# Kernel optimization log

Hardware: AMD Instinct MI355X
Metric: run time of the kernel (lower is better)

The kernel has to match this reference:

```python
import jax, jax.numpy as jnp
import numpy as np

N_NODES = 100000
N_EDGES = 3200000
D_FEAT = 128
N_LAYERS = 2

def setup_inputs() -> dict:
    key = jax.random.key(0)
    k1, k2, k3, k4 = jax.random.split(key, 4)
    x = jax.random.normal(k1, (N_NODES, D_FEAT), dtype=jnp.float32)
    edge_row = jax.random.randint(k2, (N_EDGES,), 0, N_NODES)  # destination (spmm output row)
    edge_col = jax.random.randint(k3, (N_EDGES,), 0, N_NODES)  # source node
    edge_vals = jax.random.uniform(k4, (N_EDGES,), dtype=jnp.float32)
    scalars = jnp.ones((N_LAYERS,), dtype=jnp.float32)  # per-layer learned scalar (init ones)
    return {"x": x, "edge_row": edge_row, "edge_col": edge_col,
            "edge_vals": edge_vals, "scalars": scalars}

def reference(x, edge_row, edge_col, edge_vals, scalars):
    # ScalarSGC forward with dropout p=0 (identity). Same adjacency each layer.
    for l in range(N_LAYERS):
        h = scalars[l] * x                      # scalar * x
        msg = edge_vals[:, None] * h[edge_col]  # [E, D] gather + scale
        agg = jax.ops.segment_sum(msg, edge_row, num_segments=N_NODES)  # spmm
        x = jax.nn.elu(agg)
    return x
```

## Files before the change

### kernel.cpp

```cpp
#include <hip/hip_runtime.h>
#include <math.h>
#include <stdint.h>


#define D_FEAT 128
#define D2     64
#define SCAN_TILE 1024

#define PB 256
#define PT 1024
#define RB_BITS 9
#define ROWS_PER_BUCKET 512
#define COL_BITS 17
#define CACHE_CAP 17152

__device__ __forceinline__ uint32_t f2bf(float f) {
    uint32_t u = __float_as_uint(f);
    return (u + 0x7FFFu + ((u >> 16) & 1u)) >> 16;
}
__device__ __forceinline__ float bf_lo(uint32_t w) { return __uint_as_float(w << 16); }
__device__ __forceinline__ float bf_hi(uint32_t w) { return __uint_as_float(w & 0xFFFF0000u); }

__global__ void convert_kernel(const float2* __restrict__ xin, uint32_t* __restrict__ xbf, int n2) {
    int i = blockIdx.x * blockDim.x + threadIdx.x;
    if (i < n2) {
        float2 f = xin[i];
        xbf[i] = f2bf(f.x) | (f2bf(f.y) << 16);
    }
}

__global__ __launch_bounds__(PT) void coarse_count_kernel(const int* __restrict__ row,
                                                          int* __restrict__ cnt,
                                                          int E, int nbuck) {
    __shared__ int hist[256];
    const int t = threadIdx.x;
    if (t < 256) hist[t] = 0;
    __syncthreads();
    const int stride = PB * PT;
    for (int i = blockIdx.x * PT + t; i < E; i += stride)
        atomicAdd(&hist[row[i] >> RB_BITS], 1);
    __syncthreads();
    if (t < nbuck) cnt[t * PB + blockIdx.x] = hist[t];
}

__global__ __launch_bounds__(SCAN_TILE) void scan1_kernel(const int* __restrict__ counts,
                                                          int* __restrict__ excl,
                                                          int* __restrict__ tileSums, int n) {
    __shared__ int wsum[16];
    const int tid  = threadIdx.x;
    const int lane = tid & 63;
    const int wave = tid >> 6;
    const int i    = blockIdx.x * SCAN_TILE + tid;

    int v = (i < n) ? counts[i] : 0;
    int incl = v;
    #pragma unroll
    for (int off = 1; off < 64; off <<= 1) {
        int t = __shfl_up(incl, off, 64);
        if (lane >= off) incl += t;
    }
    if (lane == 63) wsum[wave] = incl;
    __syncthreads();
    if (wave == 0) {
        int s = (lane < 16) ? wsum[lane] : 0;
        #pragma unroll
        for (int off = 1; off < 16; off <<= 1) {
            int t = __shfl_up(s, off, 64);
            if (lane >= off) s += t;
        }
        if (lane < 16) wsum[lane] = s;
    }
    __syncthreads();
    int wbase = (wave == 0) ? 0 : wsum[wave - 1];
    if (i < n) excl[i] = wbase + (incl - v);
    if (tid == 0) tileSums[blockIdx.x] = wsum[15];
}

__global__ __launch_bounds__(1024) void scan2_kernel(const int* __restrict__ tileSums,
                                                     int* __restrict__ tileBase,
                                                     int* __restrict__ total_out, int nb) {
    __shared__ int buf[1024];
    const int tid = threadIdx.x;
    int v = (tid < nb) ? tileSums[tid] : 0;
    buf[tid] = v;
    __syncthreads();
    #pragma unroll
    for (int off = 1; off < 1024; off <<= 1) {
        int t = (tid >= off) ? buf[tid - off] : 0;
        __syncthreads();
        buf[tid] += t;
        __syncthreads();
    }
    if (tid < nb) tileBase[tid] = buf[tid] - v;
    if (tid == nb - 1) *total_out = buf[tid];
}

__global__ __launch_bounds__(PT) void partition_kernel(const int* __restrict__ row,
                                                       const int* __restrict__ col,
                                                       const float* __restrict__ val,
                                                       const int* __restrict__ cnt,
                                                       const int* __restrict__ tileBase,
                                                       int2* __restrict__ pack2,
                                                       int E, int nbuck) {
    __shared__ int cur[256];
    const int t = threadIdx.x;
    if (t < nbuck) {
        int idx = t * PB + blockIdx.x;
        cur[t] = cnt[idx] + tileBase[idx >> 10];
    }
    __syncthreads();
    const int stride = PB * PT;
    for (int i = blockIdx.x * PT + t; i < E; i += stride) {
        int r = row[i];
        int pos = atomicAdd(&cur[r >> RB_BITS], 1);
        pack2[pos] = make_int2(col[i] | ((r & (ROWS_PER_BUCKET - 1)) << COL_BITS),
                               __float_as_int(val[i]));
    }
}

__global__ __launch_bounds__(1024) void fine_sort_kernel(const int* __restrict__ cnt,
                                                         const int* __restrict__ tileBase,
                                                         const int2* __restrict__ pack2,
                                                         int2* __restrict__ pack,
                                                         int* __restrict__ offsets,
                                                         int E, int N, int nbuck) {
    extern __shared__ int2 ecache[];
    __shared__ int buf[1024];
    __shared__ int cur[ROWS_PER_BUCKET];
    const int b = blockIdx.x;
    const int t = threadIdx.x;
    const int start = cnt[b << 8] + tileBase[b >> 2];
    const int end   = (b == nbuck - 1) ? E : (cnt[(b + 1) << 8] + tileBase[(b + 1) >> 2]);
    const int n  = end - start;
    const int nc = (n < CACHE_CAP) ? n : CACHE_CAP;

    for (int i = t; i < nc; i += 1024) ecache[i] = pack2[start + i];
    buf[t] = 0;
    __syncthreads();

    for (int i = t; i < n; i += 1024) {
        int key = (i < nc) ? ecache[i].x : pack2[start + i].x;
        atomicAdd(&buf[((unsigned)key) >> COL_BITS], 1);
    }
    __syncthreads();

    int v = buf[t];
    for (int off = 1; off < 1024; off <<= 1) {
        int tv = (t >= off) ? buf[t - off] : 0;
        __syncthreads();
        buf[t] += tv;
        __syncthreads();
    }
    int excl = buf[t] - v;
    if (t < ROWS_PER_BUCKET) {
        int r = (b << RB_BITS) + t;
        if (r < N) offsets[r] = start + excl;
        cur[t] = excl;
    }
    if (b == 0 && t == 0) offsets[N] = E;
    __syncthreads();

    for (int i = t; i < n; i += 1024) {
        int2 w = (i < nc) ? ecache[i] : pack2[start + i];
        int lr = ((unsigned)w.x) >> COL_BITS;
        int p = atomicAdd(&cur[lr], 1);
        pack[start + p] = make_int2(w.x & ((1 << COL_BITS) - 1), w.y);
    }
}

template <int OUT_BF16>
__global__ __launch_bounds__(256) void spmm_elu_kernel(
    const int* __restrict__ offsets, const int2* __restrict__ pack,
    const uint32_t* __restrict__ xin, void* __restrict__ xout,
    const float* __restrict__ scalars, int layer, int N) {
    const int tid = threadIdx.x;
    const int grp = tid >> 4;
    const int sub = tid & 15;
    const int r   = blockIdx.x * 16 + grp;

    int e = 0, end = 0;
    if (r < N) { e = offsets[r]; end = offsets[r + 1]; }

    const uint4* __restrict__ xin4 = (const uint4*)xin;

    float a[8];
    #pragma unroll
    for (int k = 0; k < 8; ++k) a[k] = 0.f;

    #define FMA8(W, V)                                                     \
        a[0] += (V) * bf_lo((W).x); a[1] += (V) * bf_hi((W).x);            \
        a[2] += (V) * bf_lo((W).y); a[3] += (V) * bf_hi((W).y);            \
        a[4] += (V) * bf_lo((W).z); a[5] += (V) * bf_hi((W).z);            \
        a[6] += (V) * bf_lo((W).w); a[7] += (V) * bf_hi((W).w);

    for (; e + 4 <= end; e += 4) {
        int2 p0 = pack[e], p1 = pack[e + 1], p2 = pack[e + 2], p3 = pack[e + 3];
        uint4 w0 = xin4[(((uint32_t)p0.x) << 4) + sub];
        uint4 w1 = xin4[(((uint32_t)p1.x) << 4) + sub];
        uint4 w2 = xin4[(((uint32_t)p2.x) << 4) + sub];
        uint4 w3 = xin4[(((uint32_t)p3.x) << 4) + sub];
        FMA8(w0, __int_as_float(p0.y));
        FMA8(w1, __int_as_float(p1.y));
        FMA8(w2, __int_as_float(p2.y));
        FMA8(w3, __int_as_float(p3.y));
    }
    for (; e < end; ++e) {
        int2 p = pack[e];
        uint4 w = xin4[(((uint32_t)p.x) << 4) + sub];
        FMA8(w, __int_as_float(p.y));
    }
    #undef FMA8

    const float s = scalars[layer];
    #pragma unroll
    for (int k = 0; k < 8; ++k) {
        float x = a[k] * s;
        a[k] = (x > 0.f) ? x : (expf(x) - 1.f);
    }

    if (r < N) {
        if (OUT_BF16) {
            uint4 o;
            o.x = f2bf(a[0]) | (f2bf(a[1]) << 16);
            o.y = f2bf(a[2]) | (f2bf(a[3]) << 16);
            o.z = f2bf(a[4]) | (f2bf(a[5]) << 16);
            o.w = f2bf(a[6]) | (f2bf(a[7]) << 16);
            ((uint4*)xout)[(size_t)r * 16 + sub] = o;
        } else {
            ((float4*)xout)[(size_t)r * 32 + sub * 2]     = make_float4(a[0], a[1], a[2], a[3]);
            ((float4*)xout)[(size_t)r * 32 + sub * 2 + 1] = make_float4(a[4], a[5], a[6], a[7]);
        }
    }
}

extern "C" void kernel_launch(void* const* d_in, const int* in_sizes, int n_in,
                              void* d_out, int out_size, void* d_ws, size_t ws_size,
                              hipStream_t stream) {
    const float* x         = (const float*)d_in[0];
    const int*   edge_row  = (const int*)d_in[1];
    const int*   edge_col  = (const int*)d_in[2];
    const float* edge_vals = (const float*)d_in[3];
    const float* scalars   = (const float*)d_in[4];

    const int N = in_sizes[0] / D_FEAT;
    const int E = in_sizes[1];
    const int nbuck = (N + ROWS_PER_BUCKET - 1) >> RB_BITS;
    const int M = nbuck * PB;
    const int NB = (M + SCAN_TILE - 1) / SCAN_TILE;

    char*  ws  = (char*)d_ws;
    size_t off = 0;
    auto alloc = [&](size_t bytes) -> void* {
        off = (off + 255) & ~(size_t)255;
        void* p = ws + off;
        off += bytes;
        return p;
    };
    int*      offsets  = (int*)alloc((size_t)(N + 1) * sizeof(int));
    int*      cnt      = (int*)alloc((size_t)(M + 1) * sizeof(int));
    int*      tileSums = (int*)alloc((size_t)NB * sizeof(int));
    int*      tileBase = (int*)alloc((size_t)NB * sizeof(int));
    int2*     pack2    = (int2*)alloc((size_t)E * sizeof(int2));
    int2*     pack     = (int2*)alloc((size_t)E * sizeof(int2));
    uint32_t* xbf      = (uint32_t*)alloc((size_t)N * D2 * sizeof(uint32_t));
    uint32_t* hbf      = (uint32_t*)pack2;
    (void)ws_size;

    convert_kernel<<<(N * D2 + 255) / 256, 256, 0, stream>>>((const float2*)x, xbf, N * D2);
    coarse_count_kernel<<<PB, PT, 0, stream>>>(edge_row, cnt, E, nbuck);
    scan1_kernel<<<NB, SCAN_TILE, 0, stream>>>(cnt, cnt, tileSums, M);
    scan2_kernel<<<1, 1024, 0, stream>>>(tileSums, tileBase, cnt + M, NB);
    partition_kernel<<<PB, PT, 0, stream>>>(edge_row, edge_col, edge_vals, cnt, tileBase,
                                            pack2, E, nbuck);
    fine_sort_kernel<<<nbuck, 1024, (size_t)CACHE_CAP * sizeof(int2), stream>>>(
        cnt, tileBase, pack2, pack, offsets, E, N, nbuck);

    const int nblk = (N + 15) / 16;
    spmm_elu_kernel<1><<<nblk, 256, 0, stream>>>(offsets, pack, xbf, hbf, scalars, 0, N);
    spmm_elu_kernel<0><<<nblk, 256, 0, stream>>>(offsets, pack, hbf, (void*)d_out, scalars, 1, N);
}
```

Measured before the change: 424.7 us.

## Shrink row buckets and sub-sort edges by column segment within each row

The row bucket size drops from 512 to 128 rows, which gives more fine-sort blocks and makes each bucket small enough to drop the large shared-memory edge cache. Inside each row, edges are now binned by the high bits of the source column (8 segments), so the gathers in spmm touch x in a more ordered pattern and should get better cache locality. The coarse histogram and partition shared arrays grow to 1024 entries to hold the larger bucket count. The risk is more atomic contention in the coarse phase and a re-read of pack2 from global memory.

```diff
diff --git a/kernel.cpp b/kernel.cpp
--- a/kernel.cpp
+++ b/kernel.cpp
@@ -9,10 +9,10 @@
 
 #define PB 256
 #define PT 1024
-#define RB_BITS 9
-#define ROWS_PER_BUCKET 512
+#define RB_BITS 7
+#define ROWS_PER_BUCKET 128
 #define COL_BITS 17
-#define CACHE_CAP 17152
+#define SEG_SHIFT 14
 
 __device__ __forceinline__ uint32_t f2bf(float f) {
     uint32_t u = __float_as_uint(f);
@@ -32,9 +32,9 @@
 __global__ __launch_bounds__(PT) void coarse_count_kernel(const int* __restrict__ row,
                                                           int* __restrict__ cnt,
                                                           int E, int nbuck) {
-    __shared__ int hist[256];
+    __shared__ int hist[1024];
     const int t = threadIdx.x;
-    if (t < 256) hist[t] = 0;
+    hist[t] = 0;
     __syncthreads();
     const int stride = PB * PT;
     for (int i = blockIdx.x * PT + t; i < E; i += stride)
@@ -102,7 +102,7 @@
                                                        const int* __restrict__ tileBase,
                                                        int2* __restrict__ pack2,
                                                        int E, int nbuck) {
-    __shared__ int cur[256];
+    __shared__ int cur[1024];
     const int t = threadIdx.x;
     if (t < nbuck) {
         int idx = t * PB + blockIdx.x;
@@ -124,47 +124,47 @@
                                                          int2* __restrict__ pack,
                                                          int* __restrict__ offsets,
                                                          int E, int N, int nbuck) {
-    extern __shared__ int2 ecache[];
-    __shared__ int buf[1024];
-    __shared__ int cur[ROWS_PER_BUCKET];
+    __shared__ int bins[1024];
     const int b = blockIdx.x;
     const int t = threadIdx.x;
     const int start = cnt[b << 8] + tileBase[b >> 2];
     const int end   = (b == nbuck - 1) ? E : (cnt[(b + 1) << 8] + tileBase[(b + 1) >> 2]);
     const int n  = end - start;
-    const int nc = (n < CACHE_CAP) ? n : CACHE_CAP;
-
-    for (int i = t; i < nc; i += 1024) ecache[i] = pack2[start + i];
-    buf[t] = 0;
+
+    bins[t] = 0;
     __syncthreads();
 
     for (int i = t; i < n; i += 1024) {
-        int key = (i < nc) ? ecache[i].x : pack2[start + i].x;
-        atomicAdd(&buf[((unsigned)key) >> COL_BITS], 1);
-    }
-    __syncthreads();
-
-    int v = buf[t];
+        int key = pack2[start + i].x;
+        int lr  = ((unsigned)key) >> COL_BITS;
+        int seg = (key & ((1 << COL_BITS) - 1)) >> SEG_SHIFT;
+        atomicAdd(&bins[(lr << 3) | seg], 1);
+    }
+    __syncthreads();
+
+    int v = bins[t];
     for (int off = 1; off < 1024; off <<= 1) {
-        int tv = (t >= off) ? buf[t - off] : 0;
-        __syncthreads();
-        buf[t] += tv;
-        __syncthreads();
-    }
-    int excl = buf[t] - v;
+        int tv = (t >= off) ? bins[t - off] : 0;
+        __syncthreads();
+        bins[t] += tv;
+        __syncthreads();
+    }
+    bins[t] -= v;
+    __syncthreads();
+
     if (t < ROWS_PER_BUCKET) {
         int r = (b << RB_BITS) + t;
-        if (r < N) offsets[r] = start + excl;
-        cur[t] = excl;
+        if (r < N) offsets[r] = start + bins[t << 3];
     }
     if (b == 0 && t == 0) offsets[N] = E;
     __syncthreads();
 
     for (int i = t; i < n; i += 1024) {
-        int2 w = (i < nc) ? ecache[i] : pack2[start + i];
-        int lr = ((unsigned)w.x) >> COL_BITS;
-        int p = atomicAdd(&cur[lr], 1);
-        pack[start + p] = make_int2(w.x & ((1 << COL_BITS) - 1), w.y);
+        int2 w = pack2[start + i];
+        int lr  = ((unsigned)w.x) >> COL_BITS;
+        int col = w.x & ((1 << COL_BITS) - 1);
+        int p = atomicAdd(&bins[(lr << 3) | (col >> SEG_SHIFT)], 1);
+        pack[start + p] = make_int2(col, w.y);
     }
 }
 
@@ -272,8 +272,7 @@
     scan2_kernel<<<1, 1024, 0, stream>>>(tileSums, tileBase, cnt + M, NB);
     partition_kernel<<<PB, PT, 0, stream>>>(edge_row, edge_col, edge_vals, cnt, tileBase,
                                             pack2, E, nbuck);
-    fine_sort_kernel<<<nbuck, 1024, (size_t)CACHE_CAP * sizeof(int2), stream>>>(
-        cnt, tileBase, pack2, pack, offsets, E, N, nbuck);
+    fine_sort_kernel<<<nbuck, 1024, 0, stream>>>(cnt, tileBase, pack2, pack, offsets, E, N, nbuck);
 
     const int nblk = (N + 15) / 16;
     spmm_elu_kernel<1><<<nblk, 256, 0, stream>>>(offsets, pack, xbf, hbf, scalars, 0, N);
```

Result: no change. 432.2 us (+1.8%).

## Fuse feature conversion into edge counting and slim down scan and fine sort

Applied to the files above, without the earlier changes.

Merges the float-to-bf16 conversion into the coarse row-count kernel, using float4 loads, so one launch does both jobs. The second-level scan becomes a single-wave shuffle scan instead of a 1024-thread shared-memory scan. The fine sort no longer stages edges in a large dynamic shared-memory cache and replaces its 1024-step barrier scan with a wave-shuffle scan over 512 rows. This cuts launch count and barrier overhead, but the fine sort now reads pack2 from global memory twice and scan2 assumes at most 64 tiles.

```diff
diff --git a/kernel.cpp b/kernel.cpp
--- a/kernel.cpp
+++ b/kernel.cpp
@@ -12,7 +12,6 @@
 #define RB_BITS 9
 #define ROWS_PER_BUCKET 512
 #define COL_BITS 17
-#define CACHE_CAP 17152
 
 __device__ __forceinline__ uint32_t f2bf(float f) {
     uint32_t u = __float_as_uint(f);
@@ -21,23 +20,23 @@
 __device__ __forceinline__ float bf_lo(uint32_t w) { return __uint_as_float(w << 16); }
 __device__ __forceinline__ float bf_hi(uint32_t w) { return __uint_as_float(w & 0xFFFF0000u); }
 
-__global__ void convert_kernel(const float2* __restrict__ xin, uint32_t* __restrict__ xbf, int n2) {
-    int i = blockIdx.x * blockDim.x + threadIdx.x;
-    if (i < n2) {
-        float2 f = xin[i];
-        xbf[i] = f2bf(f.x) | (f2bf(f.y) << 16);
-    }
-}
-
-__global__ __launch_bounds__(PT) void coarse_count_kernel(const int* __restrict__ row,
-                                                          int* __restrict__ cnt,
-                                                          int E, int nbuck) {
+__global__ __launch_bounds__(PT) void convert_count_kernel(const float4* __restrict__ xin,
+                                                           uint2* __restrict__ xbf, int n4,
+                                                           const int* __restrict__ row,
+                                                           int* __restrict__ cnt,
+                                                           int E, int nbuck) {
     __shared__ int hist[256];
     const int t = threadIdx.x;
     if (t < 256) hist[t] = 0;
     __syncthreads();
     const int stride = PB * PT;
-    for (int i = blockIdx.x * PT + t; i < E; i += stride)
+    const int gid = blockIdx.x * PT + t;
+    for (int i = gid; i < n4; i += stride) {
+        float4 f = xin[i];
+        xbf[i] = make_uint2(f2bf(f.x) | (f2bf(f.y) << 16),
+                            f2bf(f.z) | (f2bf(f.w) << 16));
+    }
+    for (int i = gid; i < E; i += stride)
         atomicAdd(&hist[row[i] >> RB_BITS], 1);
     __syncthreads();
     if (t < nbuck) cnt[t * PB + blockIdx.x] = hist[t];
@@ -76,23 +75,19 @@
     if (tid == 0) tileSums[blockIdx.x] = wsum[15];
 }
 
-__global__ __launch_bounds__(1024) void scan2_kernel(const int* __restrict__ tileSums,
-                                                     int* __restrict__ tileBase,
-                                                     int* __restrict__ total_out, int nb) {
-    __shared__ int buf[1024];
-    const int tid = threadIdx.x;
-    int v = (tid < nb) ? tileSums[tid] : 0;
-    buf[tid] = v;
-    __syncthreads();
-    #pragma unroll
-    for (int off = 1; off < 1024; off <<= 1) {
-        int t = (tid >= off) ? buf[tid - off] : 0;
-        __syncthreads();
-        buf[tid] += t;
-        __syncthreads();
-    }
-    if (tid < nb) tileBase[tid] = buf[tid] - v;
-    if (tid == nb - 1) *total_out = buf[tid];
+__global__ __launch_bounds__(64) void scan2_kernel(const int* __restrict__ tileSums,
+                                                   int* __restrict__ tileBase,
+                                                   int* __restrict__ total_out, int nb) {
+    const int lane = threadIdx.x;
+    int v = (lane < nb) ? tileSums[lane] : 0;
+    int incl = v;
+    #pragma unroll
+    for (int off = 1; off < 64; off <<= 1) {
+        int t = __shfl_up(incl, off, 64);
+        if (lane >= off) incl += t;
+    }
+    if (lane < nb) tileBase[lane] = incl - v;
+    if (lane == nb - 1) *total_out = incl;
 }
 
 __global__ __launch_bounds__(PT) void partition_kernel(const int* __restrict__ row,
@@ -124,44 +119,58 @@
                                                          int2* __restrict__ pack,
                                                          int* __restrict__ offsets,
                                                          int E, int N, int nbuck) {
-    extern __shared__ int2 ecache[];
-    __shared__ int buf[1024];
+    __shared__ int hist[ROWS_PER_BUCKET];
     __shared__ int cur[ROWS_PER_BUCKET];
-    const int b = blockIdx.x;
-    const int t = threadIdx.x;
+    __shared__ int wsum[8];
+    const int b    = blockIdx.x;
+    const int t    = threadIdx.x;
+    const int wave = t >> 6;
+    const int lane = t & 63;
     const int start = cnt[b << 8] + tileBase[b >> 2];
     const int end   = (b == nbuck - 1) ? E : (cnt[(b + 1) << 8] + tileBase[(b + 1) >> 2]);
-    const int n  = end - start;
-    const int nc = (n < CACHE_CAP) ? n : CACHE_CAP;
-
-    for (int i = t; i < nc; i += 1024) ecache[i] = pack2[start + i];
-    buf[t] = 0;
-    __syncthreads();
-
-    for (int i = t; i < n; i += 1024) {
-        int key = (i < nc) ? ecache[i].x : pack2[start + i].x;
-        atomicAdd(&buf[((unsigned)key) >> COL_BITS], 1);
-    }
-    __syncthreads();
-
-    int v = buf[t];
-    for (int off = 1; off < 1024; off <<= 1) {
-        int tv = (t >= off) ? buf[t - off] : 0;
-        __syncthreads();
-        buf[t] += tv;
-        __syncthreads();
-    }
-    int excl = buf[t] - v;
+    const int n = end - start;
+
+    if (t < ROWS_PER_BUCKET) hist[t] = 0;
+    __syncthreads();
+
+    for (int i = t; i < n; i += 1024)
+        atomicAdd(&hist[((unsigned)pack2[start + i].x) >> COL_BITS], 1);
+    __syncthreads();
+
+    int v = 0, incl = 0;
     if (t < ROWS_PER_BUCKET) {
+        v = hist[t];
+        incl = v;
+        #pragma unroll
+        for (int off = 1; off < 64; off <<= 1) {
+            int tv = __shfl_up(incl, off, 64);
+            if (lane >= off) incl += tv;
+        }
+        if (lane == 63) wsum[wave] = incl;
+    }
+    __syncthreads();
+    if (wave == 0) {
+        int s = (lane < 8) ? wsum[lane] : 0;
+        #pragma unroll
+        for (int off = 1; off < 8; off <<= 1) {
+            int tv = __shfl_up(s, off, 64);
+            if (lane >= off) s += tv;
+        }
+        if (lane < 8) wsum[lane] = s;
+    }
+    __syncthreads();
+    if (t < ROWS_PER_BUCKET) {
+        int base = (wave == 0) ? 0 : wsum[wave - 1];
+        int excl = base + incl - v;
+        cur[t] = excl;
         int r = (b << RB_BITS) + t;
         if (r < N) offsets[r] = start + excl;
-        cur[t] = excl;
     }
     if (b == 0 && t == 0) offsets[N] = E;
     __syncthreads();
 
     for (int i = t; i < n; i += 1024) {
-        int2 w = (i < nc) ? ecache[i] : pack2[start + i];
+        int2 w = pack2[start + i];
         int lr = ((unsigned)w.x) >> COL_BITS;
         int p = atomicAdd(&cur[lr], 1);
         pack[start + p] = make_int2(w.x & ((1 << COL_BITS) - 1), w.y);
@@ -266,14 +275,13 @@
     uint32_t* hbf      = (uint32_t*)pack2;
     (void)ws_size;
 
-    convert_kernel<<<(N * D2 + 255) / 256, 256, 0, stream>>>((const float2*)x, xbf, N * D2);
-    coarse_count_kernel<<<PB, PT, 0, stream>>>(edge_row, cnt, E, nbuck);
+    convert_count_kernel<<<PB, PT, 0, stream>>>((const float4*)x, (uint2*)xbf, N * D2 / 2,
+                                                edge_row, cnt, E, nbuck);
     scan1_kernel<<<NB, SCAN_TILE, 0, stream>>>(cnt, cnt, tileSums, M);
-    scan2_kernel<<<1, 1024, 0, stream>>>(tileSums, tileBase, cnt + M, NB);
+    scan2_kernel<<<1, 64, 0, stream>>>(tileSums, tileBase, cnt + M, NB);
     partition_kernel<<<PB, PT, 0, stream>>>(edge_row, edge_col, edge_vals, cnt, tileBase,
                                             pack2, E, nbuck);
-    fine_sort_kernel<<<nbuck, 1024, (size_t)CACHE_CAP * sizeof(int2), stream>>>(
-        cnt, tileBase, pack2, pack, offsets, E, N, nbuck);
+    fine_sort_kernel<<<nbuck, 1024, 0, stream>>>(cnt, tileBase, pack2, pack, offsets, E, N, nbuck);
 
     const int nblk = (N + 15) / 16;
     spmm_elu_kernel<1><<<nblk, 256, 0, stream>>>(offsets, pack, xbf, hbf, scalars, 0, N);
```

Result: no change. 427.1 us (+0.6%).
